# Performance work log

Hardware: AMD Instinct MI355X
Metric: run time of the kernel (lower is better)

Reference implementation:

```python
import jax, jax.numpy as jnp
import numpy as np

N_NODES = 35
N_EDGES = 1190
N_VIEWS = 6
C1_IN, C1_OUT = 1, 256
C2_IN, C2_OUT = 256, 256
C3_IN, C3_OUT = 256, 64


def _nnconv(x, edge_attr, src, dst, nn_w, nn_b, lin_w, bias, c_in, c_out):
    """PyG NNConv with aggr='mean': per-edge MLP weight, gather-matvec-scatter."""
    # per-edge weight matrices: [E, c_in, c_out]
    W = jax.nn.relu(edge_attr @ nn_w.T + nn_b).reshape(-1, c_in, c_out)
    # gather source features and apply per-edge weight: [E, c_out]
    msg = jnp.einsum('ei,eio->eo', x[src], W)
    # scatter-mean into target nodes
    agg = jax.ops.segment_sum(msg, dst, num_segments=N_NODES)
    cnt = jax.ops.segment_sum(jnp.ones((msg.shape[0],), msg.dtype), dst,
                              num_segments=N_NODES)
    agg = agg / jnp.maximum(cnt, 1.0)[:, None]
    # root transform (lin has no bias in PyG) + conv bias
    return agg + x @ lin_w.T + bias


def setup_inputs() -> dict:
    key = jax.random.key(0)
    ks = jax.random.split(key, 16)
    s = 0.05
    x = jnp.ones((N_NODES, C1_IN), jnp.float32)
    edge_attr = jax.random.uniform(ks[0], (N_EDGES, N_VIEWS), jnp.float32)
    edge_index = jax.random.randint(ks[1], (2, N_EDGES), 0, N_NODES, jnp.int32)
    inp = {
        'x': x, 'edge_attr': edge_attr, 'edge_index': edge_index,
        'nn1_w': jax.random.normal(ks[2], (C1_IN * C1_OUT, N_VIEWS), jnp.float32) * s,
        'nn1_b': jax.random.normal(ks[3], (C1_IN * C1_OUT,), jnp.float32) * s,
        'lin1_w': jax.random.normal(ks[4], (C1_OUT, C1_IN), jnp.float32) * s,
        'b1': jax.random.normal(ks[5], (C1_OUT,), jnp.float32) * s,
        'nn2_w': jax.random.normal(ks[6], (C2_IN * C2_OUT, N_VIEWS), jnp.float32) * s,
        'nn2_b': jax.random.normal(ks[7], (C2_IN * C2_OUT,), jnp.float32) * s,
        'lin2_w': jax.random.normal(ks[8], (C2_OUT, C2_IN), jnp.float32) * s,
        'b2': jax.random.normal(ks[9], (C2_OUT,), jnp.float32) * s,
        'nn3_w': jax.random.normal(ks[10], (C3_IN * C3_OUT, N_VIEWS), jnp.float32) * s,
        'nn3_b': jax.random.normal(ks[11], (C3_IN * C3_OUT,), jnp.float32) * s,
        'lin3_w': jax.random.normal(ks[12], (C3_OUT, C3_IN), jnp.float32) * s,
        'b3': jax.random.normal(ks[13], (C3_OUT,), jnp.float32) * s,
    }
    return inp


def reference(x, edge_attr, edge_index, nn1_w, nn1_b, lin1_w, b1,
              nn2_w, nn2_b, lin2_w, b2, nn3_w, nn3_b, lin3_w, b3):
    src, dst = edge_index[0], edge_index[1]
    x = jax.nn.relu(_nnconv(x, edge_attr, src, dst, nn1_w, nn1_b, lin1_w, b1, C1_IN, C1_OUT))
    x = jax.nn.relu(_nnconv(x, edge_attr, src, dst, nn2_w, nn2_b, lin2_w, b2, C2_IN, C2_OUT))
    x = jax.nn.relu(_nnconv(x, edge_attr, src, dst, nn3_w, nn3_b, lin3_w, b3, C3_IN, C3_OUT))
    # CBT: pairwise L1 distances over feature dim -> [N, N]
    # (equivalent to repeat(35,1,1) / transpose / abs / sum since N == 35)
    cbt = jnp.abs(x[None, :, :] - x[:, None, :]).sum(-1)
    return cbt
```

## Files before the change

### kernel.cpp

```cpp
#include <hip/hip_runtime.h>


#define NN 35
#define NE 1190
#define NBLK 238
#define TE2 10
#define TE3 5
#define MAXE 96

#define OFF_CNT  160
#define OFF_X1   256
#define OFF_X2   9216
#define OFF_X3   18176
#define OFF_AGG2 20480
#define OFF_AGG3 56320
#define NZERO2   22400

__global__ __launch_bounds__(64) void init_k(unsigned* bar) {
    for (int i = threadIdx.x; i < 160; i += 64) bar[i] = 0u;
}

__device__ __forceinline__ float ld_c(const float* p) {
    return __hip_atomic_load(p, __ATOMIC_RELAXED, __HIP_MEMORY_SCOPE_AGENT);
}
__device__ __forceinline__ void st_c(float* p, float v) {
    __hip_atomic_store(p, v, __ATOMIC_RELAXED, __HIP_MEMORY_SCOPE_AGENT);
}
__device__ __forceinline__ float2 ld_c2(const float* p) {
    union { double d; float2 f; } u;
    u.d = __hip_atomic_load((const double*)p, __ATOMIC_RELAXED,
                            __HIP_MEMORY_SCOPE_AGENT);
    return u.f;
}
__device__ __forceinline__ void st_c2(float* p, float2 v) {
    union { double d; float2 f; } u;
    u.f = v;
    __hip_atomic_store((double*)p, u.d, __ATOMIC_RELAXED,
                       __HIP_MEMORY_SCOPE_AGENT);
}

__device__ __forceinline__ void gbar(unsigned* bar, unsigned target) {
    __syncthreads();
    if (threadIdx.x == 0) {
        __hip_atomic_fetch_add(bar + (blockIdx.x & 7) * 16, 1u,
                               __ATOMIC_RELAXED, __HIP_MEMORY_SCOPE_AGENT);
        for (;;) {
            unsigned s = 0;
#pragma unroll
            for (int i = 0; i < 8; i++)
                s += __hip_atomic_load(bar + i * 16, __ATOMIC_RELAXED,
                                       __HIP_MEMORY_SCOPE_AGENT);
            if (s >= target) break;
            __builtin_amdgcn_s_sleep(8);
        }
        asm volatile("" ::: "memory");
    }
    __syncthreads();
}

__global__ __launch_bounds__(512) void mega_k(
    float* __restrict__ ws, const float* __restrict__ x,
    const float* __restrict__ ea, const int* __restrict__ ei,
    const float* __restrict__ w1, const float* __restrict__ b1w,
    const float* __restrict__ lin1, const float* __restrict__ b1,
    const float* __restrict__ w2, const float* __restrict__ b2w,
    const float* __restrict__ lin2, const float* __restrict__ b2,
    const float* __restrict__ w3, const float* __restrict__ b3w,
    const float* __restrict__ lin3, const float* __restrict__ b3,
    float* __restrict__ out) {
    __shared__ float smem[4096];
    unsigned* bar = (unsigned*)ws;
    const int tid = threadIdx.x;
    const int bid = blockIdx.x;

    if (bid < 140) {
        const int n = bid >> 2, och = bid & 3;
        int* elistS = (int*)smem;
        int* ecntS = (int*)smem + 96;
        float* partS = smem + 128;
        if (tid == 0) *ecntS = 0;
        __syncthreads();
        for (int e = tid; e < NE; e += 512) {
            if (ei[NE + e] == n) {
                const int p = atomicAdd(ecntS, 1);
                if (p < MAXE) elistS[p] = e;
            }
        }
        __syncthreads();
        const int deg = *ecntS;
        const int dl = deg < MAXE ? deg : MAXE;
        const int ol = tid & 63, ech = tid >> 6;
        const int o = och * 64 + ol;
        const float2* wr = (const float2*)(w1 + o * 6);
        const float2 wv0 = wr[0], wv1 = wr[1], wv2 = wr[2];
        const float bb = b1w[o];
        float a = 0.f;
        for (int k = ech; k < dl; k += 8) {
            const int e = elistS[k];
            const float2* eap = (const float2*)(ea + e * 6);
            const float2 a0 = eap[0], a1 = eap[1], a2 = eap[2];
            float d = bb;
            d = fmaf(a0.x, wv0.x, d); d = fmaf(a0.y, wv0.y, d);
            d = fmaf(a1.x, wv1.x, d); d = fmaf(a1.y, wv1.y, d);
            d = fmaf(a2.x, wv2.x, d); d = fmaf(a2.y, wv2.y, d);
            a = fmaf(x[ei[e]], fmaxf(d, 0.f), a);
        }
        partS[ech * 64 + ol] = a;
        __syncthreads();
        if (ech == 0) {
            float s = a;
#pragma unroll
            for (int p = 1; p < 8; p++) s += partS[p * 64 + ol];
            const float c = fmaxf((float)deg, 1.f);
            st_c(ws + OFF_X1 + n * 256 + o,
                 fmaxf(s / c + x[n] * lin1[o] + b1[o], 0.f));
        }
        if (och == 0 && tid == 0) st_c(ws + OFF_CNT + n, (float)deg);
    } else {
        const int idx = (bid - 140) * 512 + tid;
        if (idx < NZERO2) {
            float2 z; z.x = 0.f; z.y = 0.f;
            st_c2(ws + OFF_AGG2 + idx * 2, z);
        }
    }
    gbar(bar, NBLK * 1u);

    {
        const int eg = bid >> 1, ig = bid & 1;
        const int e0 = eg * TE2;
        const int rep = bid & 3;
        int* srcsS = (int*)smem;
        int* dstsS = (int*)smem + 16;
        float* easS = smem + 32;
        float* xsS = smem + 96;
        float* partS = smem + 1408;
        if (tid < TE2) { srcsS[tid] = ei[e0 + tid]; dstsS[tid] = ei[NE + e0 + tid]; }
        if (tid >= 64 && tid < 64 + TE2 * 6) {
            const int t = tid - 64;
            easS[t] = ea[e0 * 6 + t];
        }
        __syncthreads();
        for (int idx = tid; idx < TE2 * 64; idx += 512) {
            const int te = idx >> 6, ip = (idx & 63) * 2;
            *(float2*)&xsS[te * 128 + ip] =
                ld_c2(ws + OFF_X1 + srcsS[te] * 256 + ig * 128 + ip);
        }
        __syncthreads();
        const int o = tid & 255, ich = tid >> 8;
        float ear[TE2][6];
#pragma unroll
        for (int te = 0; te < TE2; te++)
#pragma unroll
            for (int v = 0; v < 6; v++) ear[te][v] = easS[te * 6 + v];
        float acc[TE2] = {};
        for (int ii = 0; ii < 64; ii++) {
            const int il = ich * 64 + ii;
            const int i = ig * 128 + il;
            const float* wp = w2 + (size_t)(i * 256 + o) * 6;
            const float2 wa = *(const float2*)wp;
            const float2 wb = *(const float2*)(wp + 2);
            const float2 wc = *(const float2*)(wp + 4);
            const float b = b2w[i * 256 + o];
#pragma unroll
            for (int te = 0; te < TE2; te += 2) {
                float dx = b, dy = b;
                dx = fmaf(ear[te][0], wa.x, dx); dy = fmaf(ear[te+1][0], wa.x, dy);
                dx = fmaf(ear[te][1], wa.y, dx); dy = fmaf(ear[te+1][1], wa.y, dy);
                dx = fmaf(ear[te][2], wb.x, dx); dy = fmaf(ear[te+1][2], wb.x, dy);
                dx = fmaf(ear[te][3], wb.y, dx); dy = fmaf(ear[te+1][3], wb.y, dy);
                dx = fmaf(ear[te][4], wc.x, dx); dy = fmaf(ear[te+1][4], wc.x, dy);
                dx = fmaf(ear[te][5], wc.y, dx); dy = fmaf(ear[te+1][5], wc.y, dy);
                dx = fmaxf(dx, 0.f);             dy = fmaxf(dy, 0.f);
                acc[te]   = fmaf(xsS[te * 128 + il], dx, acc[te]);
                acc[te+1] = fmaf(xsS[(te+1) * 128 + il], dy, acc[te+1]);
            }
        }
        if (ich == 1) {
#pragma unroll
            for (int te = 0; te < TE2; te++) partS[te * 256 + o] = acc[te];
        }
        __syncthreads();
        if (ich == 0) {
#pragma unroll
            for (int te = 0; te < TE2; te++)
                atomicAdd(ws + OFF_AGG2 + rep * 8960 + dstsS[te] * 256 + o,
                          acc[te] + partS[te * 256 + o]);
        }
    }
    gbar(bar, NBLK * 2u);

    if (bid < 140) {
        const int n = bid >> 2, og = bid & 3;
        float* x1S = smem;
        float* partS = smem + 256;
        float* cS = smem + 768;
        if (tid == 0) cS[0] = ld_c(ws + OFF_CNT + n);
        if (tid >= 128 && tid < 256) {
            const int ip = (tid - 128) * 2;
            *(float2*)&x1S[ip] = ld_c2(ws + OFF_X1 + n * 256 + ip);
        }
        __syncthreads();
        const int ol = tid & 63, ic = tid >> 6;
        const int o = og * 64 + ol;
        const float4* l4 = (const float4*)(lin2 + (size_t)o * 256 + ic * 32);
        const float* xs = x1S + ic * 32;
        float s = 0.f;
#pragma unroll
        for (int k = 0; k < 8; k++) {
            const float4 wv = l4[k];
            s = fmaf(wv.x, xs[k * 4], s);
            s = fmaf(wv.y, xs[k * 4 + 1], s);
            s = fmaf(wv.z, xs[k * 4 + 2], s);
            s = fmaf(wv.w, xs[k * 4 + 3], s);
        }
        partS[ic * 64 + ol] = s;
        __syncthreads();
        if (ic == 0) {
            float t = s;
#pragma unroll
            for (int p = 1; p < 8; p++) t += partS[p * 64 + ol];
            float g = 0.f;
#pragma unroll
            for (int r = 0; r < 4; r++)
                g += ld_c(ws + OFF_AGG2 + r * 8960 + n * 256 + o);
            const float c = fmaxf(cS[0], 1.f);
            st_c(ws + OFF_X2 + n * 256 + o, fmaxf(g / c + t + b2[o], 0.f));
        }
    }
    gbar(bar, NBLK * 3u);

    {
        const int e0 = bid * TE3;
        const int rep = bid & 3;
        int* srcsS = (int*)smem;
        int* dstsS = (int*)smem + 8;
        float* easS = smem + 16;
        float* xsS = smem + 64;
        float* partS = smem + 1344;
        if (tid < TE3) { srcsS[tid] = ei[e0 + tid]; dstsS[tid] = ei[NE + e0 + tid]; }
        if (tid >= 64 && tid < 64 + TE3 * 6) {
            const int t = tid - 64;
            easS[t] = ea[e0 * 6 + t];
        }
        __syncthreads();
        for (int idx = tid; idx < TE3 * 128; idx += 512) {
            const int te = idx >> 7, ip = (idx & 127) * 2;
            *(float2*)&xsS[te * 256 + ip] =
                ld_c2(ws + OFF_X2 + srcsS[te] * 256 + ip);
        }
        __syncthreads();
        const int o3 = tid & 63, ic = tid >> 6;
        float ear[TE3][6];
#pragma unroll
        for (int te = 0; te < TE3; te++)
#pragma unroll
            for (int v = 0; v < 6; v++) ear[te][v] = easS[te * 6 + v];
        float acc[TE3] = {};
        for (int ii = 0; ii < 32; ii++) {
            const int i = ic * 32 + ii;
            const float* wp = w3 + (size_t)(i * 64 + o3) * 6;
            const float2 wa = *(const float2*)wp;
            const float2 wb = *(const float2*)(wp + 2);
            const float2 wc = *(const float2*)(wp + 4);
            const float b = b3w[i * 64 + o3];
#pragma unroll
            for (int te = 0; te < TE3; te++) {
                float d = b;
                d = fmaf(ear[te][0], wa.x, d);
                d = fmaf(ear[te][1], wa.y, d);
                d = fmaf(ear[te][2], wb.x, d);
                d = fmaf(ear[te][3], wb.y, d);
                d = fmaf(ear[te][4], wc.x, d);
                d = fmaf(ear[te][5], wc.y, d);
                acc[te] = fmaf(xsS[te * 256 + i], fmaxf(d, 0.f), acc[te]);
            }
        }
        if (ic > 0) {
#pragma unroll
            for (int te = 0; te < TE3; te++)
                partS[(ic - 1) * 320 + te * 64 + o3] = acc[te];
        }
        __syncthreads();
        if (ic == 0) {
#pragma unroll
            for (int te = 0; te < TE3; te++) {
                float s = acc[te];
#pragma unroll
                for (int p = 0; p < 7; p++) s += partS[p * 320 + te * 64 + o3];
                atomicAdd(ws + OFF_AGG3 + rep * 2240 + dstsS[te] * 64 + o3, s);
            }
        }
    }
    gbar(bar, NBLK * 4u);

    if (bid >= NN) return;
    {
        const int n = bid;
        float* x2S = smem;
        float* partS = smem + 256;
        float* cS = smem + 768;
        if (tid == 0) cS[0] = ld_c(ws + OFF_CNT + n);
        if (tid >= 128 && tid < 256) {
            const int ip = (tid - 128) * 2;
            *(float2*)&x2S[ip] = ld_c2(ws + OFF_X2 + n * 256 + ip);
        }
        __syncthreads();
        const int o3 = tid & 63, ic = tid >> 6;
        const float4* l4 = (const float4*)(lin3 + (size_t)o3 * 256 + ic * 32);
        const float* xs = x2S + ic * 32;
        float s = 0.f;
#pragma unroll
        for (int k = 0; k < 8; k++) {
            const float4 wv = l4[k];
            s = fmaf(wv.x, xs[k * 4], s);
            s = fmaf(wv.y, xs[k * 4 + 1], s);
            s = fmaf(wv.z, xs[k * 4 + 2], s);
            s = fmaf(wv.w, xs[k * 4 + 3], s);
        }
        partS[ic * 64 + o3] = s;
        __syncthreads();
        if (ic == 0) {
            float t = s;
#pragma unroll
            for (int p = 1; p < 8; p++) t += partS[p * 64 + o3];
            float g = 0.f;
#pragma unroll
            for (int r = 0; r < 4; r++)
                g += ld_c(ws + OFF_AGG3 + r * 2240 + n * 64 + o3);
            const float c = fmaxf(cS[0], 1.f);
            st_c(ws + OFF_X3 + n * 64 + o3, fmaxf(g / c + t + b3[o3], 0.f));
        }
        __syncthreads();
        if (tid == 0) {
            unsigned* flag = bar + 128;
            __hip_atomic_fetch_add(flag, 1u, __ATOMIC_RELAXED,
                                   __HIP_MEMORY_SCOPE_AGENT);
            while (__hip_atomic_load(flag, __ATOMIC_RELAXED,
                                     __HIP_MEMORY_SCOPE_AGENT) < NN)
                __builtin_amdgcn_s_sleep(4);
            asm volatile("" ::: "memory");
        }
        __syncthreads();
        float* sx = smem;
        for (int idx = tid; idx < NN * 32; idx += 512)
            *(float2*)&sx[idx * 2] = ld_c2(ws + OFF_X3 + idx * 2);
        __syncthreads();
        const int f = tid & 63, jg = tid >> 6;
        const float xi = sx[bid * 64 + f];
        for (int j = jg; j < NN; j += 8) {
            float d = fabsf(xi - sx[j * 64 + f]);
#pragma unroll
            for (int off = 32; off > 0; off >>= 1) d += __shfl_xor(d, off);
            if (f == 0) out[bid * NN + j] = d;
        }
    }
}

extern "C" void kernel_launch(void* const* d_in, const int* in_sizes, int n_in,
                              void* d_out, int out_size, void* d_ws, size_t ws_size,
                              hipStream_t stream) {
    (void)in_sizes; (void)n_in; (void)out_size; (void)ws_size;
    const float* x    = (const float*)d_in[0];
    const float* ea   = (const float*)d_in[1];
    const int*   ei   = (const int*)d_in[2];
    const float* nn1w = (const float*)d_in[3];
    const float* nn1b = (const float*)d_in[4];
    const float* lin1 = (const float*)d_in[5];
    const float* b1   = (const float*)d_in[6];
    const float* nn2w = (const float*)d_in[7];
    const float* nn2b = (const float*)d_in[8];
    const float* lin2 = (const float*)d_in[9];
    const float* b2   = (const float*)d_in[10];
    const float* nn3w = (const float*)d_in[11];
    const float* nn3b = (const float*)d_in[12];
    const float* lin3 = (const float*)d_in[13];
    const float* b3   = (const float*)d_in[14];

    float* ws = (float*)d_ws;
    init_k<<<1, 64, 0, stream>>>((unsigned*)d_ws);
    mega_k<<<NBLK, 512, 0, stream>>>(ws, x, ea, ei, nn1w, nn1b, lin1, b1,
                                     nn2w, nn2b, lin2, b2, nn3w, nn3b,
                                     lin3, b3, (float*)d_out);
}
```

Measured before the change: 155.7 us.

## Double grid size and split edge-MLP phases across output halves

Doubles the persistent grid from 238 to 476 blocks, giving each block in the layer-2 and layer-3 edge phases half of the output channels and a shorter inner-dimension loop. Reductions across thread groups now sum more partials in shared memory, and the software grid barrier is spread over 16 counters instead of 8. The aim is more active waves on the GPU to hide weight-load latency, and launch_bounds(512,4) caps registers to allow co-residency. The cost is more barrier participants, more redundant x/edge loads per block, and possible register spills.

```diff
diff --git a/kernel.cpp b/kernel.cpp
--- a/kernel.cpp
+++ b/kernel.cpp
@@ -3,21 +3,21 @@
 
 #define NN 35
 #define NE 1190
-#define NBLK 238
+#define NBLK 476
 #define TE2 10
 #define TE3 5
 #define MAXE 96
 
-#define OFF_CNT  160
-#define OFF_X1   256
-#define OFF_X2   9216
-#define OFF_X3   18176
-#define OFF_AGG2 20480
-#define OFF_AGG3 56320
+#define OFF_CNT  320
+#define OFF_X1   384
+#define OFF_X2   9344
+#define OFF_X3   18304
+#define OFF_AGG2 20608
+#define OFF_AGG3 56448
 #define NZERO2   22400
 
 __global__ __launch_bounds__(64) void init_k(unsigned* bar) {
-    for (int i = threadIdx.x; i < 160; i += 64) bar[i] = 0u;
+    for (int i = threadIdx.x; i < 320; i += 64) bar[i] = 0u;
 }
 
 __device__ __forceinline__ float ld_c(const float* p) {
@@ -42,12 +42,12 @@
 __device__ __forceinline__ void gbar(unsigned* bar, unsigned target) {
     __syncthreads();
     if (threadIdx.x == 0) {
-        __hip_atomic_fetch_add(bar + (blockIdx.x & 7) * 16, 1u,
+        __hip_atomic_fetch_add(bar + (blockIdx.x & 15) * 16, 1u,
                                __ATOMIC_RELAXED, __HIP_MEMORY_SCOPE_AGENT);
         for (;;) {
             unsigned s = 0;
 #pragma unroll
-            for (int i = 0; i < 8; i++)
+            for (int i = 0; i < 16; i++)
                 s += __hip_atomic_load(bar + i * 16, __ATOMIC_RELAXED,
                                        __HIP_MEMORY_SCOPE_AGENT);
             if (s >= target) break;
@@ -58,7 +58,7 @@
     __syncthreads();
 }
 
-__global__ __launch_bounds__(512) void mega_k(
+__global__ __launch_bounds__(512, 4) void mega_k(
     float* __restrict__ ws, const float* __restrict__ x,
     const float* __restrict__ ea, const int* __restrict__ ei,
     const float* __restrict__ w1, const float* __restrict__ b1w,
@@ -68,7 +68,7 @@
     const float* __restrict__ w3, const float* __restrict__ b3w,
     const float* __restrict__ lin3, const float* __restrict__ b3,
     float* __restrict__ out) {
-    __shared__ float smem[4096];
+    __shared__ float smem[5376];
     unsigned* bar = (unsigned*)ws;
     const int tid = threadIdx.x;
     const int bid = blockIdx.x;
@@ -116,7 +116,7 @@
                  fmaxf(s / c + x[n] * lin1[o] + b1[o], 0.f));
         }
         if (och == 0 && tid == 0) st_c(ws + OFF_CNT + n, (float)deg);
-    } else {
+    } else if (bid < 184) {
         const int idx = (bid - 140) * 512 + tid;
         if (idx < NZERO2) {
             float2 z; z.x = 0.f; z.y = 0.f;
@@ -126,9 +126,10 @@
     gbar(bar, NBLK * 1u);
 
     {
-        const int eg = bid >> 1, ig = bid & 1;
+        const int eg = bid >> 2, sub = bid & 3;
+        const int ig = sub >> 1, og = sub & 1;
         const int e0 = eg * TE2;
-        const int rep = bid & 3;
+        const int rep = eg & 3;
         int* srcsS = (int*)smem;
         int* dstsS = (int*)smem + 16;
         float* easS = smem + 32;
@@ -146,15 +147,16 @@
                 ld_c2(ws + OFF_X1 + srcsS[te] * 256 + ig * 128 + ip);
         }
         __syncthreads();
-        const int o = tid & 255, ich = tid >> 8;
+        const int ol = tid & 127, ich = tid >> 7;
+        const int o = og * 128 + ol;
         float ear[TE2][6];
 #pragma unroll
         for (int te = 0; te < TE2; te++)
 #pragma unroll
             for (int v = 0; v < 6; v++) ear[te][v] = easS[te * 6 + v];
         float acc[TE2] = {};
-        for (int ii = 0; ii < 64; ii++) {
-            const int il = ich * 64 + ii;
+        for (int ii = 0; ii < 32; ii++) {
+            const int il = ich * 32 + ii;
             const int i = ig * 128 + il;
             const float* wp = w2 + (size_t)(i * 256 + o) * 6;
             const float2 wa = *(const float2*)wp;
@@ -175,16 +177,20 @@
                 acc[te+1] = fmaf(xsS[(te+1) * 128 + il], dy, acc[te+1]);
             }
         }
-        if (ich == 1) {
-#pragma unroll
-            for (int te = 0; te < TE2; te++) partS[te * 256 + o] = acc[te];
+        if (ich > 0) {
+#pragma unroll
+            for (int te = 0; te < TE2; te++)
+                partS[(ich - 1) * 1280 + te * 128 + ol] = acc[te];
         }
         __syncthreads();
         if (ich == 0) {
 #pragma unroll
-            for (int te = 0; te < TE2; te++)
-                atomicAdd(ws + OFF_AGG2 + rep * 8960 + dstsS[te] * 256 + o,
-                          acc[te] + partS[te * 256 + o]);
+            for (int te = 0; te < TE2; te++) {
+                float s = acc[te] + partS[te * 128 + ol]
+                        + partS[1280 + te * 128 + ol]
+                        + partS[2560 + te * 128 + ol];
+                atomicAdd(ws + OFF_AGG2 + rep * 8960 + dstsS[te] * 256 + o, s);
+            }
         }
     }
     gbar(bar, NBLK * 2u);
@@ -230,8 +236,9 @@
     gbar(bar, NBLK * 3u);
 
     {
-        const int e0 = bid * TE3;
-        const int rep = bid & 3;
+        const int eg = bid >> 1, oh = bid & 1;
+        const int e0 = eg * TE3;
+        const int rep = eg & 3;
         int* srcsS = (int*)smem;
         int* dstsS = (int*)smem + 8;
         float* easS = smem + 16;
@@ -249,15 +256,16 @@
                 ld_c2(ws + OFF_X2 + srcsS[te] * 256 + ip);
         }
         __syncthreads();
-        const int o3 = tid & 63, ic = tid >> 6;
+        const int o3l = tid & 31, ic = tid >> 5;
+        const int o3 = oh * 32 + o3l;
         float ear[TE3][6];
 #pragma unroll
         for (int te = 0; te < TE3; te++)
 #pragma unroll
             for (int v = 0; v < 6; v++) ear[te][v] = easS[te * 6 + v];
         float acc[TE3] = {};
-        for (int ii = 0; ii < 32; ii++) {
-            const int i = ic * 32 + ii;
+        for (int ii = 0; ii < 16; ii++) {
+            const int i = ic * 16 + ii;
             const float* wp = w3 + (size_t)(i * 64 + o3) * 6;
             const float2 wa = *(const float2*)wp;
             const float2 wb = *(const float2*)(wp + 2);
@@ -278,7 +286,7 @@
         if (ic > 0) {
 #pragma unroll
             for (int te = 0; te < TE3; te++)
-                partS[(ic - 1) * 320 + te * 64 + o3] = acc[te];
+                partS[(ic - 1) * 160 + te * 32 + o3l] = acc[te];
         }
         __syncthreads();
         if (ic == 0) {
@@ -286,7 +294,7 @@
             for (int te = 0; te < TE3; te++) {
                 float s = acc[te];
 #pragma unroll
-                for (int p = 0; p < 7; p++) s += partS[p * 320 + te * 64 + o3];
+                for (int p = 0; p < 15; p++) s += partS[p * 160 + te * 32 + o3l];
                 atomicAdd(ws + OFF_AGG3 + rep * 2240 + dstsS[te] * 64 + o3, s);
             }
         }
@@ -332,7 +340,7 @@
         }
         __syncthreads();
         if (tid == 0) {
-            unsigned* flag = bar + 128;
+            unsigned* flag = bar + 256;
             __hip_atomic_fetch_add(flag, 1u, __ATOMIC_RELAXED,
                                    __HIP_MEMORY_SCOPE_AGENT);
             while (__hip_atomic_load(flag, __ATOMIC_RELAXED,
```

Measured after the change: 158.5 us. No clear change (+1.8%).
